# Kernel optimization log

Measured on AMD Instinct MI355X. Metric: run time of the kernel, lower is better.

## Reference

```python
import jax, jax.numpy as jnp
import numpy as np

N = 50000
E = 800000
IN_CH = 128
HID = 32
HEADS = 4
OUT_CH = 40
LEAKY = 0.2
BN_EPS = 1e-5


def _gat_layer(x, src, dst, W, a_src, a_dst, b, n_nodes, concat):
    # x: [N, F_in], W: [F_in, H*C], a_src/a_dst: [H, C], b: [H*C] or [C]
    H, C = a_src.shape
    h = (x @ W).reshape(n_nodes, H, C)                      # [N, H, C]
    e_s = jnp.einsum('nhc,hc->nh', h, a_src)                # [N, H]
    e_d = jnp.einsum('nhc,hc->nh', h, a_dst)                # [N, H]
    e = e_s[src] + e_d[dst]                                 # [E, H]
    e = jnp.where(e > 0, e, LEAKY * e)                      # LeakyReLU
    # segment softmax over incoming edges of each destination node
    m = jax.ops.segment_max(e, dst, num_segments=n_nodes)   # [N, H]
    ex = jnp.exp(e - m[dst])
    s = jax.ops.segment_sum(ex, dst, num_segments=n_nodes)  # [N, H]
    alpha = ex / s[dst]                                     # [E, H]
    out = jax.ops.segment_sum(h[src] * alpha[:, :, None], dst,
                              num_segments=n_nodes)         # [N, H, C]
    out = out.reshape(n_nodes, H * C) if concat else out.mean(axis=1)
    return out + b


def setup_inputs() -> dict:
    key = jax.random.key(0)
    ks = jax.random.split(key, 16)
    d1 = HEADS * HID  # 128
    inp = {
        'x': jax.random.normal(ks[0], (N, IN_CH), dtype=jnp.float32),
        'edge_index': jax.random.randint(ks[1], (2, E), 0, N, dtype=jnp.int64),
        # conv1 params (heads=4, concat)
        'W1': jax.random.normal(ks[2], (IN_CH, d1), dtype=jnp.float32) * 0.1,
        'a1_src': jax.random.normal(ks[3], (HEADS, HID), dtype=jnp.float32) * 0.1,
        'a1_dst': jax.random.normal(ks[4], (HEADS, HID), dtype=jnp.float32) * 0.1,
        'b1': jnp.zeros((d1,), dtype=jnp.float32),
        # BatchNorm1d(128) in eval mode
        'bn_gamma': jnp.ones((d1,), dtype=jnp.float32),
        'bn_beta': jnp.zeros((d1,), dtype=jnp.float32),
        'bn_mean': jax.random.normal(ks[5], (d1,), dtype=jnp.float32) * 0.1,
        'bn_var': jax.random.uniform(ks[6], (d1,), minval=0.5, maxval=1.5, dtype=jnp.float32),
        # conv2 params (heads=1, concat=False)
        'W2': jax.random.normal(ks[7], (d1, OUT_CH), dtype=jnp.float32) * 0.1,
        'a2_src': jax.random.normal(ks[8], (1, OUT_CH), dtype=jnp.float32) * 0.1,
        'a2_dst': jax.random.normal(ks[9], (1, OUT_CH), dtype=jnp.float32) * 0.1,
        'b2': jnp.zeros((OUT_CH,), dtype=jnp.float32),
    }
    return inp


def reference(x, edge_index, W1, a1_src, a1_dst, b1, bn_gamma, bn_beta,
              bn_mean, bn_var, W2, a2_src, a2_dst, b2):
    n = x.shape[0]
    loops = jnp.arange(n, dtype=edge_index.dtype)
    src = jnp.concatenate([edge_index[0], loops])  # PyG GATConv adds self-loops
    dst = jnp.concatenate([edge_index[1], loops])
    h = _gat_layer(x, src, dst, W1, a1_src, a1_dst, b1, n, concat=True)
    h = (h - bn_mean) / jnp.sqrt(bn_var + BN_EPS) * bn_gamma + bn_beta  # BN eval
    h = jax.nn.elu(h)
    # dropout is identity in eval mode
    out = _gat_layer(h, src, dst, W2, a2_src, a2_dst, b2, n, concat=False)
    return jax.nn.log_softmax(out, axis=1)
```

## Files before the change

kernel.cpp:

```cpp
#include <hip/hip_runtime.h>
#include <hip/hip_bf16.h>
#include <math.h>

#define NN 50000
#define NE 800000
#define ETOT (NE + NN)
#define LEAKY 0.2f
#define BN_EPS 1e-5f

#define NB 256
#define BSZ 196
#define NBB 128
#define EPB ((ETOT + NBB - 1) / NBB)
#define PREPB 80

#define BN1 144
#define BN2 48

typedef unsigned short u16;
typedef unsigned int u32;
typedef short s16;
typedef __attribute__((ext_vector_type(8))) short bf16x8;
typedef __attribute__((ext_vector_type(4))) float f32x4;

__device__ __forceinline__ float bf2f(u32 u) {
    union { u32 i; float f; } x; x.i = u << 16; return x.f;
}
__device__ __forceinline__ float bf2f_lo(u32 u) {
    union { u32 i; float f; } x; x.i = u << 16; return x.f;
}
__device__ __forceinline__ float bf2f_hi(u32 u) {
    union { u32 i; float f; } x; x.i = u & 0xffff0000u; return x.f;
}
__device__ __forceinline__ u16 f2bf(float f) {
    __hip_bfloat16 b = __float2bfloat16(f);
    return *reinterpret_cast<u16*>(&b);
}

__global__ __launch_bounds__(256) void k_binA_prep(
        const int* __restrict__ ei, int* __restrict__ cnt,
        const float* __restrict__ W1, const float* __restrict__ a1s,
        const float* __restrict__ a1d, const float* __restrict__ W2,
        const float* __restrict__ a2s, const float* __restrict__ a2d,
        u16* __restrict__ Wt1, u16* __restrict__ Wt2) {
    if (blockIdx.x < NBB) {
        __shared__ int hist[NB];
        int t = threadIdx.x;
        for (int i = t; i < NB; i += 256) hist[i] = 0;
        __syncthreads();
        int e0 = blockIdx.x * EPB, e1 = min(e0 + EPB, ETOT);
        for (int e = e0 + t; e < e1; e += 256) {
            int dst = (e < NE) ? ei[NE + e] : (e - NE);
            atomicAdd(&hist[dst / BSZ], 1);
        }
        __syncthreads();
        for (int b = t; b < NB; b += 256) cnt[b * NBB + blockIdx.x] = hist[b];
    } else {
        int tid = (blockIdx.x - NBB) * 256 + threadIdx.x;
        int nth = PREPB * 256;
        for (int idx = tid; idx < BN1 * 128; idx += nth) {
            int n = idx >> 7, k = idx & 127;
            float v = 0.f;
            if (n < 128) v = W1[k * 128 + n];
            else if (n < 132) {
                int h = n - 128; float s = 0.f;
                for (int c = 0; c < 32; ++c) s += W1[k * 128 + h * 32 + c] * a1s[h * 32 + c];
                v = s;
            } else if (n < 136) {
                int h = n - 132; float s = 0.f;
                for (int c = 0; c < 32; ++c) s += W1[k * 128 + h * 32 + c] * a1d[h * 32 + c];
                v = s;
            }
            Wt1[idx] = f2bf(v);
        }
        for (int idx = tid; idx < BN2 * 128; idx += nth) {
            int n = idx >> 7, k = idx & 127;
            float v = 0.f;
            if (n < 40) v = W2[k * 40 + n];
            else if (n == 40) { float s = 0.f; for (int c = 0; c < 40; ++c) s += W2[k * 40 + c] * a2s[c]; v = s; }
            else if (n == 41) { float s = 0.f; for (int c = 0; c < 40; ++c) s += W2[k * 40 + c] * a2d[c]; v = s; }
            Wt2[idx] = f2bf(v);
        }
    }
}

__global__ __launch_bounds__(1024) void k_scanONE(const int* __restrict__ in,
                                                  int* __restrict__ out) {
    __shared__ int sums[1024];
    int t = threadIdx.x;
    int4 loc[8];
    const int4* ip = (const int4*)(in + t * 32);
    int s = 0;
    #pragma unroll
    for (int i = 0; i < 8; ++i) {
        loc[i] = ip[i];
        s += loc[i].x + loc[i].y + loc[i].z + loc[i].w;
    }
    sums[t] = s;
    __syncthreads();
    for (int off = 1; off < 1024; off <<= 1) {
        int u = (t >= off) ? sums[t - off] : 0;
        __syncthreads();
        sums[t] += u;
        __syncthreads();
    }
    int run = (t == 0) ? 0 : sums[t - 1];
    int* op = out + t * 32;
    #pragma unroll
    for (int i = 0; i < 8; ++i) {
        op[i * 4 + 0] = run; run += loc[i].x;
        op[i * 4 + 1] = run; run += loc[i].y;
        op[i * 4 + 2] = run; run += loc[i].z;
        op[i * 4 + 3] = run; run += loc[i].w;
    }
}

__global__ __launch_bounds__(256) void k_binB(const int* __restrict__ ei,
                                              const int* __restrict__ excl,
                                              u32* __restrict__ packed) {
    __shared__ int cur[NB];
    int t = threadIdx.x;
    for (int b = t; b < NB; b += 256) cur[b] = excl[b * NBB + blockIdx.x];
    __syncthreads();
    int e0 = blockIdx.x * EPB, e1 = min(e0 + EPB, ETOT);
    for (int e = e0 + t; e < e1; e += 256) {
        int src, dst;
        if (e < NE) { src = ei[e]; dst = ei[NE + e]; }
        else        { src = e - NE; dst = e - NE; }
        int pos = atomicAdd(&cur[dst / BSZ], 1);
        packed[pos] = ((u32)src << 16) | (u32)dst;
    }
}

__global__ __launch_bounds__(256) void k_binC(const u32* __restrict__ packed,
                                              const int* __restrict__ excl,
                                              int* __restrict__ offsets,
                                              int* __restrict__ ssrc) {
    __shared__ int hist[256];
    __shared__ int sc[256];
    __shared__ int cur[256];
    int b = blockIdx.x, t = threadIdx.x;
    int n0 = b * BSZ;
    int base = excl[b * NBB];
    int next = (b < NB - 1) ? excl[(b + 1) * NBB] : ETOT;
    int total = next - base;
    hist[t] = 0;
    __syncthreads();
    for (int i = t; i < total; i += 256) {
        int dst = (int)(packed[base + i] & 0xffffu);
        atomicAdd(&hist[dst - n0], 1);
    }
    __syncthreads();
    int v = hist[t];
    sc[t] = v;
    __syncthreads();
    #pragma unroll
    for (int off = 1; off < 256; off <<= 1) {
        int u = (t >= off) ? sc[t - off] : 0;
        __syncthreads();
        sc[t] += u;
        __syncthreads();
    }
    int exl = sc[t] - v;
    int node = n0 + t;
    if (t <= BSZ && node <= NN) {
        if (t < BSZ || node == NN) offsets[node] = base + exl;
    }
    cur[t] = exl;
    __syncthreads();
    for (int i = t; i < total; i += 256) {
        u32 pv = packed[base + i];
        int dst = (int)(pv & 0xffffu);
        int pos = atomicAdd(&cur[dst - n0], 1);
        ssrc[base + pos] = (int)(pv >> 16);
    }
}

__global__ __launch_bounds__(256) void k_mm1(const float* __restrict__ x,
                                             const u16* __restrict__ Wt1,
                                             u16* __restrict__ h1b,
                                             float* __restrict__ es1,
                                             float* __restrict__ ed1) {
    __shared__ __align__(16) s16 As[128 * 128];
    __shared__ __align__(16) s16 Bs[BN1 * 128];
    int t = threadIdx.x;
    int row0 = blockIdx.x * 128;
    #pragma unroll
    for (int i = 0; i < 16; ++i) {
        int c = t + i * 256;
        int r = c >> 5, k0 = (c & 31) * 4;
        float4 v = make_float4(0.f, 0.f, 0.f, 0.f);
        int row = row0 + r;
        if (row < NN) v = *(const float4*)&x[(size_t)row * 128 + k0];
        u16 pk[4] = {f2bf(v.x), f2bf(v.y), f2bf(v.z), f2bf(v.w)};
        int byte = (r * 256 + k0 * 2) ^ ((r & 7) << 4);
        *(uint2*)((char*)As + byte) = *(uint2*)pk;
    }
    #pragma unroll
    for (int i = 0; i < 9; ++i) {
        int c = t + i * 256;
        int n = c >> 4, k0 = (c & 15) * 8;
        uint4 v = *(const uint4*)&Wt1[n * 128 + k0];
        int byte = (n * 256 + k0 * 2) ^ ((n & 7) << 4);
        *(uint4*)((char*)Bs + byte) = v;
    }
    __syncthreads();
    int wave = t >> 6, lane = t & 63;
    int lr = lane & 15, lq = lane >> 4;
    int wrow = wave * 32;
    f32x4 acc[2][9];
    #pragma unroll
    for (int a = 0; a < 2; ++a)
        #pragma unroll
        for (int b = 0; b < 9; ++b) acc[a][b] = (f32x4){0.f, 0.f, 0.f, 0.f};
    #pragma unroll
    for (int ks = 0; ks < 4; ++ks) {
        int kb = ks * 32 + lq * 8;
        bf16x8 af[2];
        #pragma unroll
        for (int rb = 0; rb < 2; ++rb) {
            int r = wrow + rb * 16 + lr;
            int byte = (r * 256 + kb * 2) ^ ((r & 7) << 4);
            af[rb] = *(bf16x8*)((char*)As + byte);
        }
        #pragma unroll
        for (int cb = 0; cb < 9; ++cb) {
            int n = cb * 16 + lr;
            int byte = (n * 256 + kb * 2) ^ ((n & 7) << 4);
            bf16x8 bfr = *(bf16x8*)((char*)Bs + byte);
            acc[0][cb] = __builtin_amdgcn_mfma_f32_16x16x32_bf16(af[0], bfr, acc[0][cb], 0, 0, 0);
            acc[1][cb] = __builtin_amdgcn_mfma_f32_16x16x32_bf16(af[1], bfr, acc[1][cb], 0, 0, 0);
        }
    }
    #pragma unroll
    for (int rb = 0; rb < 2; ++rb) {
        #pragma unroll
        for (int cb = 0; cb < 9; ++cb) {
            #pragma unroll
            for (int r = 0; r < 4; ++r) {
                int row = row0 + wrow + rb * 16 + lq * 4 + r;
                int col = cb * 16 + lr;
                if (row < NN) {
                    float v = acc[rb][cb][r];
                    if (col < 128) h1b[(size_t)row * 128 + col] = f2bf(v);
                    else if (col < 132) es1[row * 4 + (col - 128)] = v;
                    else if (col < 136) ed1[row * 4 + (col - 132)] = v;
                }
            }
        }
    }
}

__global__ __launch_bounds__(256) void k_mm2(const u16* __restrict__ hbnb,
                                             const u16* __restrict__ Wt2,
                                             u16* __restrict__ h2b,
                                             float* __restrict__ ed2) {
    __shared__ __align__(16) s16 As[128 * 128];
    __shared__ __align__(16) s16 Bs[BN2 * 128];
    int t = threadIdx.x;
    int row0 = blockIdx.x * 128;
    #pragma unroll
    for (int i = 0; i < 8; ++i) {
        int c = t + i * 256;
        int r = c >> 4, k0 = (c & 15) * 8;
        uint4 v = make_uint4(0, 0, 0, 0);
        int row = row0 + r;
        if (row < NN) v = *(const uint4*)&hbnb[(size_t)row * 128 + k0];
        int byte = (r * 256 + k0 * 2) ^ ((r & 7) << 4);
        *(uint4*)((char*)As + byte) = v;
    }
    #pragma unroll
    for (int i = 0; i < 3; ++i) {
        int c = t + i * 256;
        int n = c >> 4, k0 = (c & 15) * 8;
        uint4 v = *(const uint4*)&Wt2[n * 128 + k0];
        int byte = (n * 256 + k0 * 2) ^ ((n & 7) << 4);
        *(uint4*)((char*)Bs + byte) = v;
    }
    __syncthreads();
    int wave = t >> 6, lane = t & 63;
    int lr = lane & 15, lq = lane >> 4;
    int wrow = wave * 32;
    f32x4 acc[2][3];
    #pragma unroll
    for (int a = 0; a < 2; ++a)
        #pragma unroll
        for (int b = 0; b < 3; ++b) acc[a][b] = (f32x4){0.f, 0.f, 0.f, 0.f};
    #pragma unroll
    for (int ks = 0; ks < 4; ++ks) {
        int kb = ks * 32 + lq * 8;
        bf16x8 af[2];
        #pragma unroll
        for (int rb = 0; rb < 2; ++rb) {
            int r = wrow + rb * 16 + lr;
            int byte = (r * 256 + kb * 2) ^ ((r & 7) << 4);
            af[rb] = *(bf16x8*)((char*)As + byte);
        }
        #pragma unroll
        for (int cb = 0; cb < 3; ++cb) {
            int n = cb * 16 + lr;
            int byte = (n * 256 + kb * 2) ^ ((n & 7) << 4);
            bf16x8 bfr = *(bf16x8*)((char*)Bs + byte);
            acc[0][cb] = __builtin_amdgcn_mfma_f32_16x16x32_bf16(af[0], bfr, acc[0][cb], 0, 0, 0);
            acc[1][cb] = __builtin_amdgcn_mfma_f32_16x16x32_bf16(af[1], bfr, acc[1][cb], 0, 0, 0);
        }
    }
    #pragma unroll
    for (int rb = 0; rb < 2; ++rb) {
        #pragma unroll
        for (int cb = 0; cb < 3; ++cb) {
            #pragma unroll
            for (int r = 0; r < 4; ++r) {
                int row = row0 + wrow + rb * 16 + lq * 4 + r;
                int col = cb * 16 + lr;
                if (row < NN) {
                    float v = acc[rb][cb][r];
                    if (col <= 40) {
                        h2b[(size_t)row * 64 + col] = f2bf(v);
                    } else {
                        if (col == 41) ed2[row] = v;
                        h2b[(size_t)row * 64 + col] = 0;
                    }
                }
            }
        }
    }
}

__global__ __launch_bounds__(256) void k_agg1(
        const u16* __restrict__ h1b, const float* __restrict__ es,
        const float* __restrict__ ed, const int* __restrict__ offsets,
        const int* __restrict__ ssrc, const float* __restrict__ b1,
        const float* __restrict__ gamma, const float* __restrict__ beta,
        const float* __restrict__ mean, const float* __restrict__ var,
        u16* __restrict__ hbnb) {
    __shared__ float wlds[4][64][4];
    int wv = threadIdx.x >> 6;
    int node = blockIdx.x * 4 + wv;
    if (node >= NN) return;
    int l = threadIdx.x & 63;
    int g = l >> 4;
    int c16 = l & 15;
    int h = c16 >> 2;
    int p0 = offsets[node], p1 = offsets[node + 1];
    float4 ed4 = *(const float4*)&ed[(size_t)node * 4];
    float4 sw4 = make_float4(0.f, 0.f, 0.f, 0.f);
    float acc[8];
    #pragma unroll
    for (int i = 0; i < 8; ++i) acc[i] = 0.f;
    for (int base = p0; base < p1; base += 64) {
        int cnt = min(64, p1 - base);
        int myidx = (l < cnt) ? ssrc[base + l] : 0;
        float4 w4 = make_float4(0.f, 0.f, 0.f, 0.f);
        if (l < cnt) {
            float4 e4 = *(const float4*)&es[(size_t)myidx * 4];
            float tv;
            tv = e4.x + ed4.x; tv = tv > 0.f ? tv : LEAKY * tv; w4.x = __expf(tv);
            tv = e4.y + ed4.y; tv = tv > 0.f ? tv : LEAKY * tv; w4.y = __expf(tv);
            tv = e4.z + ed4.z; tv = tv > 0.f ? tv : LEAKY * tv; w4.z = __expf(tv);
            tv = e4.w + ed4.w; tv = tv > 0.f ? tv : LEAKY * tv; w4.w = __expf(tv);
        }
        *(float4*)&wlds[wv][l][0] = w4;
        sw4.x += w4.x; sw4.y += w4.y; sw4.z += w4.z; sw4.w += w4.w;
        __builtin_amdgcn_wave_barrier();
        for (int j = 0; j < cnt; j += 16) {
            int e0 = j + g, e1 = j + 4 + g, e2 = j + 8 + g, e3 = j + 12 + g;
            int c0v = min(e0, cnt - 1), c1v = min(e1, cnt - 1);
            int c2v = min(e2, cnt - 1), c3v = min(e3, cnt - 1);
            int s0 = __shfl(myidx, c0v);
            int s1 = __shfl(myidx, c1v);
            int s2 = __shfl(myidx, c2v);
            int s3 = __shfl(myidx, c3v);
            float x0 = (e0 < cnt) ? wlds[wv][c0v][h] : 0.f;
            float x1 = (e1 < cnt) ? wlds[wv][c1v][h] : 0.f;
            float x2 = (e2 < cnt) ? wlds[wv][c2v][h] : 0.f;
            float x3 = (e3 < cnt) ? wlds[wv][c3v][h] : 0.f;
            uint4 r0 = *(const uint4*)&h1b[(size_t)s0 * 128 + c16 * 8];
            uint4 r1 = *(const uint4*)&h1b[(size_t)s1 * 128 + c16 * 8];
            uint4 r2 = *(const uint4*)&h1b[(size_t)s2 * 128 + c16 * 8];
            uint4 r3 = *(const uint4*)&h1b[(size_t)s3 * 128 + c16 * 8];
            acc[0] = fmaf(x0, bf2f_lo(r0.x), acc[0]);
            acc[1] = fmaf(x0, bf2f_hi(r0.x), acc[1]);
            acc[2] = fmaf(x0, bf2f_lo(r0.y), acc[2]);
            acc[3] = fmaf(x0, bf2f_hi(r0.y), acc[3]);
            acc[4] = fmaf(x0, bf2f_lo(r0.z), acc[4]);
            acc[5] = fmaf(x0, bf2f_hi(r0.z), acc[5]);
            acc[6] = fmaf(x0, bf2f_lo(r0.w), acc[6]);
            acc[7] = fmaf(x0, bf2f_hi(r0.w), acc[7]);
            acc[0] = fmaf(x1, bf2f_lo(r1.x), acc[0]);
            acc[1] = fmaf(x1, bf2f_hi(r1.x), acc[1]);
            acc[2] = fmaf(x1, bf2f_lo(r1.y), acc[2]);
            acc[3] = fmaf(x1, bf2f_hi(r1.y), acc[3]);
            acc[4] = fmaf(x1, bf2f_lo(r1.z), acc[4]);
            acc[5] = fmaf(x1, bf2f_hi(r1.z), acc[5]);
            acc[6] = fmaf(x1, bf2f_lo(r1.w), acc[6]);
            acc[7] = fmaf(x1, bf2f_hi(r1.w), acc[7]);
            acc[0] = fmaf(x2, bf2f_lo(r2.x), acc[0]);
            acc[1] = fmaf(x2, bf2f_hi(r2.x), acc[1]);
            acc[2] = fmaf(x2, bf2f_lo(r2.y), acc[2]);
            acc[3] = fmaf(x2, bf2f_hi(r2.y), acc[3]);
            acc[4] = fmaf(x2, bf2f_lo(r2.z), acc[4]);
            acc[5] = fmaf(x2, bf2f_hi(r2.z), acc[5]);
            acc[6] = fmaf(x2, bf2f_lo(r2.w), acc[6]);
            acc[7] = fmaf(x2, bf2f_hi(r2.w), acc[7]);
            acc[0] = fmaf(x3, bf2f_lo(r3.x), acc[0]);
            acc[1] = fmaf(x3, bf2f_hi(r3.x), acc[1]);
            acc[2] = fmaf(x3, bf2f_lo(r3.y), acc[2]);
            acc[3] = fmaf(x3, bf2f_hi(r3.y), acc[3]);
            acc[4] = fmaf(x3, bf2f_lo(r3.z), acc[4]);
            acc[5] = fmaf(x3, bf2f_hi(r3.z), acc[5]);
            acc[6] = fmaf(x3, bf2f_lo(r3.w), acc[6]);
            acc[7] = fmaf(x3, bf2f_hi(r3.w), acc[7]);
        }
    }
    #pragma unroll
    for (int i = 0; i < 8; ++i) {
        acc[i] += __shfl_xor(acc[i], 16);
        acc[i] += __shfl_xor(acc[i], 32);
    }
    #pragma unroll
    for (int off = 1; off < 64; off <<= 1) {
        sw4.x += __shfl_xor(sw4.x, off);
        sw4.y += __shfl_xor(sw4.y, off);
        sw4.z += __shfl_xor(sw4.z, off);
        sw4.w += __shfl_xor(sw4.w, off);
    }
    if (g == 0) {
        float s = (h == 0) ? sw4.x : (h == 1) ? sw4.y : (h == 2) ? sw4.z : sw4.w;
        float inv = 1.f / s;
        int c0 = c16 * 8;
        float4 b1a = *(const float4*)&b1[c0],    b1b = *(const float4*)&b1[c0 + 4];
        float4 mna = *(const float4*)&mean[c0],  mnb = *(const float4*)&mean[c0 + 4];
        float4 vra = *(const float4*)&var[c0],   vrb = *(const float4*)&var[c0 + 4];
        float4 gma = *(const float4*)&gamma[c0], gmb = *(const float4*)&gamma[c0 + 4];
        float4 bta = *(const float4*)&beta[c0],  btb = *(const float4*)&beta[c0 + 4];
        float bv[8] = {b1a.x, b1a.y, b1a.z, b1a.w, b1b.x, b1b.y, b1b.z, b1b.w};
        float mn[8] = {mna.x, mna.y, mna.z, mna.w, mnb.x, mnb.y, mnb.z, mnb.w};
        float vr[8] = {vra.x, vra.y, vra.z, vra.w, vrb.x, vrb.y, vrb.z, vrb.w};
        float gm[8] = {gma.x, gma.y, gma.z, gma.w, gmb.x, gmb.y, gmb.z, gmb.w};
        float bt[8] = {bta.x, bta.y, bta.z, bta.w, btb.x, btb.y, btb.z, btb.w};
        u16 pk[8];
        #pragma unroll
        for (int i = 0; i < 8; ++i) {
            float o = acc[i] * inv + bv[i];
            o = (o - mn[i]) * rsqrtf(vr[i] + BN_EPS) * gm[i] + bt[i];
            o = o > 0.f ? o : __expf(o) - 1.f;
            pk[i] = f2bf(o);
        }
        *(uint4*)&hbnb[(size_t)node * 128 + c0] = *(uint4*)pk;
    }
}

__global__ __launch_bounds__(256) void k_agg2(
        const u16* __restrict__ h2b, const float* __restrict__ ed,
        const int* __restrict__ offsets, const int* __restrict__ ssrc,
        const float* __restrict__ b2, float* __restrict__ out) {
    __shared__ float wlds[4][64];
    int wv = threadIdx.x >> 6;
    int node = blockIdx.x * 4 + wv;
    if (node >= NN) return;
    int l = threadIdx.x & 63;
    int g = l >> 3;
    int c8 = l & 7;
    int p0 = offsets[node], p1 = offsets[node + 1];
    float edv = ed[node];
    float swacc = 0.f;
    float acc[8];
    #pragma unroll
    for (int i = 0; i < 8; ++i) acc[i] = 0.f;
    for (int base = p0; base < p1; base += 64) {
        int cnt = min(64, p1 - base);
        int myidx = (l < cnt) ? ssrc[base + l] : 0;
        float mw = 0.f;
        if (l < cnt) {
            float esv = bf2f((u32)h2b[(size_t)myidx * 64 + 40]);
            float e = esv + edv;
            e = e > 0.f ? e : LEAKY * e;
            mw = __expf(e);
        }
        wlds[wv][l] = mw;
        swacc += mw;
        __builtin_amdgcn_wave_barrier();
        for (int j = 0; j < cnt; j += 32) {
            int e0 = j + g, e1 = j + 8 + g, e2 = j + 16 + g, e3 = j + 24 + g;
            int c0v = min(e0, cnt - 1), c1v = min(e1, cnt - 1);
            int c2v = min(e2, cnt - 1), c3v = min(e3, cnt - 1);
            int s0 = __shfl(myidx, c0v);
            int s1 = __shfl(myidx, c1v);
            int s2 = __shfl(myidx, c2v);
            int s3 = __shfl(myidx, c3v);
            float x0 = (e0 < cnt) ? wlds[wv][c0v] : 0.f;
            float x1 = (e1 < cnt) ? wlds[wv][c1v] : 0.f;
            float x2 = (e2 < cnt) ? wlds[wv][c2v] : 0.f;
            float x3 = (e3 < cnt) ? wlds[wv][c3v] : 0.f;
            uint4 r0 = *(const uint4*)&h2b[(size_t)s0 * 64 + c8 * 8];
            uint4 r1 = *(const uint4*)&h2b[(size_t)s1 * 64 + c8 * 8];
            uint4 r2 = *(const uint4*)&h2b[(size_t)s2 * 64 + c8 * 8];
            uint4 r3 = *(const uint4*)&h2b[(size_t)s3 * 64 + c8 * 8];
            acc[0] = fmaf(x0, bf2f_lo(r0.x), acc[0]);
            acc[1] = fmaf(x0, bf2f_hi(r0.x), acc[1]);
            acc[2] = fmaf(x0, bf2f_lo(r0.y), acc[2]);
            acc[3] = fmaf(x0, bf2f_hi(r0.y), acc[3]);
            acc[4] = fmaf(x0, bf2f_lo(r0.z), acc[4]);
            acc[5] = fmaf(x0, bf2f_hi(r0.z), acc[5]);
            acc[6] = fmaf(x0, bf2f_lo(r0.w), acc[6]);
            acc[7] = fmaf(x0, bf2f_hi(r0.w), acc[7]);
            acc[0] = fmaf(x1, bf2f_lo(r1.x), acc[0]);
            acc[1] = fmaf(x1, bf2f_hi(r1.x), acc[1]);
            acc[2] = fmaf(x1, bf2f_lo(r1.y), acc[2]);
            acc[3] = fmaf(x1, bf2f_hi(r1.y), acc[3]);
            acc[4] = fmaf(x1, bf2f_lo(r1.z), acc[4]);
            acc[5] = fmaf(x1, bf2f_hi(r1.z), acc[5]);
            acc[6] = fmaf(x1, bf2f_lo(r1.w), acc[6]);
            acc[7] = fmaf(x1, bf2f_hi(r1.w), acc[7]);
            acc[0] = fmaf(x2, bf2f_lo(r2.x), acc[0]);
            acc[1] = fmaf(x2, bf2f_hi(r2.x), acc[1]);
            acc[2] = fmaf(x2, bf2f_lo(r2.y), acc[2]);
            acc[3] = fmaf(x2, bf2f_hi(r2.y), acc[3]);
            acc[4] = fmaf(x2, bf2f_lo(r2.z), acc[4]);
            acc[5] = fmaf(x2, bf2f_hi(r2.z), acc[5]);
            acc[6] = fmaf(x2, bf2f_lo(r2.w), acc[6]);
            acc[7] = fmaf(x2, bf2f_hi(r2.w), acc[7]);
            acc[0] = fmaf(x3, bf2f_lo(r3.x), acc[0]);
            acc[1] = fmaf(x3, bf2f_hi(r3.x), acc[1]);
            acc[2] = fmaf(x3, bf2f_lo(r3.y), acc[2]);
            acc[3] = fmaf(x3, bf2f_hi(r3.y), acc[3]);
            acc[4] = fmaf(x3, bf2f_lo(r3.z), acc[4]);
            acc[5] = fmaf(x3, bf2f_hi(r3.z), acc[5]);
            acc[6] = fmaf(x3, bf2f_lo(r3.w), acc[6]);
            acc[7] = fmaf(x3, bf2f_hi(r3.w), acc[7]);
        }
    }
    #pragma unroll
    for (int i = 0; i < 8; ++i) {
        acc[i] += __shfl_xor(acc[i], 8);
        acc[i] += __shfl_xor(acc[i], 16);
        acc[i] += __shfl_xor(acc[i], 32);
    }
    float s = swacc;
    #pragma unroll
    for (int off = 1; off < 64; off <<= 1) s += __shfl_xor(s, off);
    float inv = 1.f / s;
    bool valid = (c8 < 5);
    int c0 = c8 * 8;
    float v[8];
    float m8 = -1e30f;
    if (valid) {
        float4 b2a = *(const float4*)&b2[c0];
        float4 b2b = *(const float4*)&b2[c0 + 4];
        float bv[8] = {b2a.x, b2a.y, b2a.z, b2a.w, b2b.x, b2b.y, b2b.z, b2b.w};
        #pragma unroll
        for (int i = 0; i < 8; ++i) {
            v[i] = acc[i] * inv + bv[i];
            m8 = fmaxf(m8, v[i]);
        }
    }
    m8 = fmaxf(m8, __shfl_xor(m8, 1));
    m8 = fmaxf(m8, __shfl_xor(m8, 2));
    m8 = fmaxf(m8, __shfl_xor(m8, 4));
    float ex = 0.f;
    if (valid) {
        #pragma unroll
        for (int i = 0; i < 8; ++i) ex += __expf(v[i] - m8);
    }
    ex += __shfl_xor(ex, 1);
    ex += __shfl_xor(ex, 2);
    ex += __shfl_xor(ex, 4);
    if (g == 0 && valid) {
        float lg = m8 + __logf(ex);
        float4 o0 = make_float4(v[0] - lg, v[1] - lg, v[2] - lg, v[3] - lg);
        float4 o1 = make_float4(v[4] - lg, v[5] - lg, v[6] - lg, v[7] - lg);
        *(float4*)&out[(size_t)node * 40 + c0] = o0;
        *(float4*)&out[(size_t)node * 40 + c0 + 4] = o1;
    }
}

extern "C" void kernel_launch(void* const* d_in, const int* in_sizes, int n_in,
                              void* d_out, int out_size, void* d_ws, size_t ws_size,
                              hipStream_t stream) {
    const float* x   = (const float*)d_in[0];
    const int*   ei  = (const int*)d_in[1];
    const float* W1  = (const float*)d_in[2];
    const float* a1s = (const float*)d_in[3];
    const float* a1d = (const float*)d_in[4];
    const float* b1  = (const float*)d_in[5];
    const float* bng = (const float*)d_in[6];
    const float* bnb = (const float*)d_in[7];
    const float* bnm = (const float*)d_in[8];
    const float* bnv = (const float*)d_in[9];
    const float* W2  = (const float*)d_in[10];
    const float* a2s = (const float*)d_in[11];
    const float* a2d = (const float*)d_in[12];
    const float* b2  = (const float*)d_in[13];
    float* out = (float*)d_out;

    char* ws = (char*)d_ws;
    size_t off = 0;
    auto alloc = [&](size_t bytes) -> void* {
        void* p = ws + off;
        off = (off + bytes + 255) & ~(size_t)255;
        return p;
    };
    int*   cntb     = (int*)alloc((size_t)NB * NBB * 4);
    int*   excl     = (int*)alloc((size_t)NB * NBB * 4);
    int*   offsets  = (int*)alloc((size_t)(NN + 1) * 4);
    u32*   packed   = (u32*)alloc((size_t)ETOT * 4);
    int*   ssrc     = (int*)alloc((size_t)ETOT * 4);
    u16*   Wt1      = (u16*)alloc((size_t)BN1 * 128 * 2);
    u16*   Wt2      = (u16*)alloc((size_t)BN2 * 128 * 2);
    u16*   h1b      = (u16*)alloc((size_t)NN * 128 * 2);
    float* es1      = (float*)alloc((size_t)NN * 4 * 4);
    float* ed1      = (float*)alloc((size_t)NN * 4 * 4);
    u16*   hbnb     = (u16*)alloc((size_t)NN * 128 * 2);
    u16*   h2b      = (u16*)alloc((size_t)NN * 64 * 2);
    float* ed2      = (float*)alloc((size_t)NN * 4);

    k_binA_prep<<<NBB + PREPB, 256, 0, stream>>>(ei, cntb, W1, a1s, a1d,
                                                 W2, a2s, a2d, Wt1, Wt2);
    k_scanONE<<<1, 1024, 0, stream>>>(cntb, excl);
    k_binB<<<NBB, 256, 0, stream>>>(ei, excl, packed);
    k_binC<<<NB, 256, 0, stream>>>(packed, excl, offsets, ssrc);
    k_mm1<<<(NN + 127) / 128, 256, 0, stream>>>(x, Wt1, h1b, es1, ed1);
    k_agg1<<<(NN + 3) / 4, 256, 0, stream>>>(h1b, es1, ed1, offsets, ssrc,
                                             b1, bng, bnb, bnm, bnv, hbnb);
    k_mm2<<<(NN + 127) / 128, 256, 0, stream>>>(hbnb, Wt2, h2b, ed2);
    k_agg2<<<(NN + 3) / 4, 256, 0, stream>>>(h2b, ed2, offsets, ssrc, b2, out);
}
```

Baseline: 143.2 us.

## Panel-split layer-1 features and shrink sorted source indices to 16-bit

Layer-1 features are now written by the first GEMM in 8 column panels of 16 channels each (panel-major layout), and the first aggregation kernel launches 8x more blocks, each handling one panel for 4 nodes. This keeps each panel's gather working set (50000 nodes x 32 bytes) small enough to stay cache-resident while edges are gathered randomly. Sorted source indices are also stored as u16 instead of int, halving their traffic. The cost is that each edge's index, attention score and exponential are recomputed once per panel (8x redundant), a longer cross-lane reduction, and fewer useful lanes per gather.

```diff
diff --git a/kernel.cpp b/kernel.cpp
--- a/kernel.cpp
+++ b/kernel.cpp
@@ -135,7 +135,7 @@
 __global__ __launch_bounds__(256) void k_binC(const u32* __restrict__ packed,
                                               const int* __restrict__ excl,
                                               int* __restrict__ offsets,
-                                              int* __restrict__ ssrc) {
+                                              u16* __restrict__ ssrc) {
     __shared__ int hist[256];
     __shared__ int sc[256];
     __shared__ int cur[256];
@@ -172,13 +172,13 @@
         u32 pv = packed[base + i];
         int dst = (int)(pv & 0xffffu);
         int pos = atomicAdd(&cur[dst - n0], 1);
-        ssrc[base + pos] = (int)(pv >> 16);
+        ssrc[base + pos] = (u16)(pv >> 16);
     }
 }
 
 __global__ __launch_bounds__(256) void k_mm1(const float* __restrict__ x,
                                              const u16* __restrict__ Wt1,
-                                             u16* __restrict__ h1b,
+                                             u16* __restrict__ h1p,
                                              float* __restrict__ es1,
                                              float* __restrict__ ed1) {
     __shared__ __align__(16) s16 As[128 * 128];
@@ -242,7 +242,10 @@
                 int col = cb * 16 + lr;
                 if (row < NN) {
                     float v = acc[rb][cb][r];
-                    if (col < 128) h1b[(size_t)row * 128 + col] = f2bf(v);
+                    if (col < 128) {
+                        int p = col >> 4, cc = col & 15;
+                        h1p[(size_t)p * NN * 16 + (size_t)row * 16 + cc] = f2bf(v);
+                    }
                     else if (col < 132) es1[row * 4 + (col - 128)] = v;
                     else if (col < 136) ed1[row * 4 + (col - 132)] = v;
                 }
@@ -328,57 +331,49 @@
 }
 
 __global__ __launch_bounds__(256) void k_agg1(
-        const u16* __restrict__ h1b, const float* __restrict__ es,
+        const u16* __restrict__ h1p, const float* __restrict__ es,
         const float* __restrict__ ed, const int* __restrict__ offsets,
-        const int* __restrict__ ssrc, const float* __restrict__ b1,
+        const u16* __restrict__ ssrc, const float* __restrict__ b1,
         const float* __restrict__ gamma, const float* __restrict__ beta,
         const float* __restrict__ mean, const float* __restrict__ var,
         u16* __restrict__ hbnb) {
-    __shared__ float wlds[4][64][4];
+    __shared__ float wlds[4][64];
     int wv = threadIdx.x >> 6;
-    int node = blockIdx.x * 4 + wv;
+    int panel = blockIdx.x & 7;
+    int node = (blockIdx.x >> 3) * 4 + wv;
     if (node >= NN) return;
     int l = threadIdx.x & 63;
-    int g = l >> 4;
-    int c16 = l & 15;
-    int h = c16 >> 2;
+    int g = l >> 1;
+    int c2 = l & 1;
+    int head = panel >> 1;
     int p0 = offsets[node], p1 = offsets[node + 1];
-    float4 ed4 = *(const float4*)&ed[(size_t)node * 4];
-    float4 sw4 = make_float4(0.f, 0.f, 0.f, 0.f);
+    float edh = ed[node * 4 + head];
+    const u16* hp = h1p + (size_t)panel * NN * 16;
+    float swacc = 0.f;
     float acc[8];
     #pragma unroll
     for (int i = 0; i < 8; ++i) acc[i] = 0.f;
     for (int base = p0; base < p1; base += 64) {
         int cnt = min(64, p1 - base);
-        int myidx = (l < cnt) ? ssrc[base + l] : 0;
-        float4 w4 = make_float4(0.f, 0.f, 0.f, 0.f);
+        int myidx = (l < cnt) ? (int)ssrc[base + l] : 0;
+        float w = 0.f;
         if (l < cnt) {
-            float4 e4 = *(const float4*)&es[(size_t)myidx * 4];
-            float tv;
-            tv = e4.x + ed4.x; tv = tv > 0.f ? tv : LEAKY * tv; w4.x = __expf(tv);
-            tv = e4.y + ed4.y; tv = tv > 0.f ? tv : LEAKY * tv; w4.y = __expf(tv);
-            tv = e4.z + ed4.z; tv = tv > 0.f ? tv : LEAKY * tv; w4.z = __expf(tv);
-            tv = e4.w + ed4.w; tv = tv > 0.f ? tv : LEAKY * tv; w4.w = __expf(tv);
-        }
-        *(float4*)&wlds[wv][l][0] = w4;
-        sw4.x += w4.x; sw4.y += w4.y; sw4.z += w4.z; sw4.w += w4.w;
+            float e = es[myidx * 4 + head] + edh;
+            e = e > 0.f ? e : LEAKY * e;
+            w = __expf(e);
+        }
+        wlds[wv][l] = w;
+        swacc += w;
         __builtin_amdgcn_wave_barrier();
-        for (int j = 0; j < cnt; j += 16) {
-            int e0 = j + g, e1 = j + 4 + g, e2 = j + 8 + g, e3 = j + 12 + g;
+        for (int j = 0; j < cnt; j += 64) {
+            int e0 = j + g, e1 = j + 32 + g;
             int c0v = min(e0, cnt - 1), c1v = min(e1, cnt - 1);
-            int c2v = min(e2, cnt - 1), c3v = min(e3, cnt - 1);
             int s0 = __shfl(myidx, c0v);
             int s1 = __shfl(myidx, c1v);
-            int s2 = __shfl(myidx, c2v);
-            int s3 = __shfl(myidx, c3v);
-            float x0 = (e0 < cnt) ? wlds[wv][c0v][h] : 0.f;
-            float x1 = (e1 < cnt) ? wlds[wv][c1v][h] : 0.f;
-            float x2 = (e2 < cnt) ? wlds[wv][c2v][h] : 0.f;
-            float x3 = (e3 < cnt) ? wlds[wv][c3v][h] : 0.f;
-            uint4 r0 = *(const uint4*)&h1b[(size_t)s0 * 128 + c16 * 8];
-            uint4 r1 = *(const uint4*)&h1b[(size_t)s1 * 128 + c16 * 8];
-            uint4 r2 = *(const uint4*)&h1b[(size_t)s2 * 128 + c16 * 8];
-            uint4 r3 = *(const uint4*)&h1b[(size_t)s3 * 128 + c16 * 8];
+            float x0 = (e0 < cnt) ? wlds[wv][c0v] : 0.f;
+            float x1 = (e1 < cnt) ? wlds[wv][c1v] : 0.f;
+            uint4 r0 = *(const uint4*)&hp[(size_t)s0 * 16 + c2 * 8];
+            uint4 r1 = *(const uint4*)&hp[(size_t)s1 * 16 + c2 * 8];
             acc[0] = fmaf(x0, bf2f_lo(r0.x), acc[0]);
             acc[1] = fmaf(x0, bf2f_hi(r0.x), acc[1]);
             acc[2] = fmaf(x0, bf2f_lo(r0.y), acc[2]);
@@ -395,40 +390,22 @@
             acc[5] = fmaf(x1, bf2f_hi(r1.z), acc[5]);
             acc[6] = fmaf(x1, bf2f_lo(r1.w), acc[6]);
             acc[7] = fmaf(x1, bf2f_hi(r1.w), acc[7]);
-            acc[0] = fmaf(x2, bf2f_lo(r2.x), acc[0]);
-            acc[1] = fmaf(x2, bf2f_hi(r2.x), acc[1]);
-            acc[2] = fmaf(x2, bf2f_lo(r2.y), acc[2]);
-            acc[3] = fmaf(x2, bf2f_hi(r2.y), acc[3]);
-            acc[4] = fmaf(x2, bf2f_lo(r2.z), acc[4]);
-            acc[5] = fmaf(x2, bf2f_hi(r2.z), acc[5]);
-            acc[6] = fmaf(x2, bf2f_lo(r2.w), acc[6]);
-            acc[7] = fmaf(x2, bf2f_hi(r2.w), acc[7]);
-            acc[0] = fmaf(x3, bf2f_lo(r3.x), acc[0]);
-            acc[1] = fmaf(x3, bf2f_hi(r3.x), acc[1]);
-            acc[2] = fmaf(x3, bf2f_lo(r3.y), acc[2]);
-            acc[3] = fmaf(x3, bf2f_hi(r3.y), acc[3]);
-            acc[4] = fmaf(x3, bf2f_lo(r3.z), acc[4]);
-            acc[5] = fmaf(x3, bf2f_hi(r3.z), acc[5]);
-            acc[6] = fmaf(x3, bf2f_lo(r3.w), acc[6]);
-            acc[7] = fmaf(x3, bf2f_hi(r3.w), acc[7]);
         }
     }
     #pragma unroll
     for (int i = 0; i < 8; ++i) {
+        acc[i] += __shfl_xor(acc[i], 2);
+        acc[i] += __shfl_xor(acc[i], 4);
+        acc[i] += __shfl_xor(acc[i], 8);
         acc[i] += __shfl_xor(acc[i], 16);
         acc[i] += __shfl_xor(acc[i], 32);
     }
-    #pragma unroll
-    for (int off = 1; off < 64; off <<= 1) {
-        sw4.x += __shfl_xor(sw4.x, off);
-        sw4.y += __shfl_xor(sw4.y, off);
-        sw4.z += __shfl_xor(sw4.z, off);
-        sw4.w += __shfl_xor(sw4.w, off);
-    }
-    if (g == 0) {
-        float s = (h == 0) ? sw4.x : (h == 1) ? sw4.y : (h == 2) ? sw4.z : sw4.w;
+    float s = swacc;
+    #pragma unroll
+    for (int off = 1; off < 64; off <<= 1) s += __shfl_xor(s, off);
+    if (l < 2) {
         float inv = 1.f / s;
-        int c0 = c16 * 8;
+        int c0 = panel * 16 + c2 * 8;
         float4 b1a = *(const float4*)&b1[c0],    b1b = *(const float4*)&b1[c0 + 4];
         float4 mna = *(const float4*)&mean[c0],  mnb = *(const float4*)&mean[c0 + 4];
         float4 vra = *(const float4*)&var[c0],   vrb = *(const float4*)&var[c0 + 4];
@@ -453,7 +430,7 @@
 
 __global__ __launch_bounds__(256) void k_agg2(
         const u16* __restrict__ h2b, const float* __restrict__ ed,
-        const int* __restrict__ offsets, const int* __restrict__ ssrc,
+        const int* __restrict__ offsets, const u16* __restrict__ ssrc,
         const float* __restrict__ b2, float* __restrict__ out) {
     __shared__ float wlds[4][64];
     int wv = threadIdx.x >> 6;
@@ -470,7 +447,7 @@
     for (int i = 0; i < 8; ++i) acc[i] = 0.f;
     for (int base = p0; base < p1; base += 64) {
         int cnt = min(64, p1 - base);
-        int myidx = (l < cnt) ? ssrc[base + l] : 0;
+        int myidx = (l < cnt) ? (int)ssrc[base + l] : 0;
         float mw = 0.f;
         if (l < cnt) {
             float esv = bf2f((u32)h2b[(size_t)myidx * 64 + 40]);
@@ -605,10 +582,10 @@
     int*   excl     = (int*)alloc((size_t)NB * NBB * 4);
     int*   offsets  = (int*)alloc((size_t)(NN + 1) * 4);
     u32*   packed   = (u32*)alloc((size_t)ETOT * 4);
-    int*   ssrc     = (int*)alloc((size_t)ETOT * 4);
+    u16*   ssrc     = (u16*)alloc((size_t)ETOT * 2);
     u16*   Wt1      = (u16*)alloc((size_t)BN1 * 128 * 2);
     u16*   Wt2      = (u16*)alloc((size_t)BN2 * 128 * 2);
-    u16*   h1b      = (u16*)alloc((size_t)NN * 128 * 2);
+    u16*   h1p      = (u16*)alloc((size_t)NN * 128 * 2);
     float* es1      = (float*)alloc((size_t)NN * 4 * 4);
     float* ed1      = (float*)alloc((size_t)NN * 4 * 4);
     u16*   hbnb     = (u16*)alloc((size_t)NN * 128 * 2);
@@ -620,9 +597,9 @@
     k_scanONE<<<1, 1024, 0, stream>>>(cntb, excl);
     k_binB<<<NBB, 256, 0, stream>>>(ei, excl, packed);
     k_binC<<<NB, 256, 0, stream>>>(packed, excl, offsets, ssrc);
-    k_mm1<<<(NN + 127) / 128, 256, 0, stream>>>(x, Wt1, h1b, es1, ed1);
-    k_agg1<<<(NN + 3) / 4, 256, 0, stream>>>(h1b, es1, ed1, offsets, ssrc,
-                                             b1, bng, bnb, bnm, bnv, hbnb);
+    k_mm1<<<(NN + 127) / 128, 256, 0, stream>>>(x, Wt1, h1p, es1, ed1);
+    k_agg1<<<((NN + 3) / 4) * 8, 256, 0, stream>>>(h1p, es1, ed1, offsets, ssrc,
+                                                   b1, bng, bnb, bnm, bnv, hbnb);
     k_mm2<<<(NN + 127) / 128, 256, 0, stream>>>(hbnb, Wt2, h2b, ed2);
     k_agg2<<<(NN + 3) / 4, 256, 0, stream>>>(h2b, ed2, offsets, ssrc, b2, out);
 }
```

After: 302.7 us. 111% more time.
